# Optimization experiments

Measured on AMD Instinct MI355X. Metric: run time of the kernel, lower is better.

Reference implementation:

```python
import jax, jax.numpy as jnp
import numpy as np

N = 100000   # nodes
E = 1600000  # edges
R = 4        # relations (bond types)
D_IN = 38    # atom feature dim
H = 64       # hidden dim
G = 1000     # graphs in batch
O = 1        # output tasks


def layer_norm(h, g, b):
    mu = h.mean(-1, keepdims=True)
    var = ((h - mu) ** 2).mean(-1, keepdims=True)
    return (h - mu) / jnp.sqrt(var + 1e-5) * g + b


def rgcn_conv(x, src, dst, etype, W, root_w, bias):
    # PyG RGCNConv with aggr='mean': per-relation mean of neighbor features,
    # then per-relation linear transform (mean commutes with the linear map),
    # plus root transform and bias.
    msg = x[src]                                   # [E, F] gather (memory-bound)
    seg = dst * R + etype                          # fused (node, relation) segment id
    sums = jax.ops.segment_sum(msg, seg, num_segments=N * R)          # [N*R, F]
    cnt = jax.ops.segment_sum(jnp.ones((msg.shape[0],), x.dtype), seg,
                              num_segments=N * R)                     # [N*R]
    mean = sums / jnp.maximum(cnt, 1.0)[:, None]
    mean = mean.reshape(N, R, x.shape[-1])         # [N, R, F]
    return jnp.einsum('nri,rio->no', mean, W) + x @ root_w + bias


def setup_inputs() -> dict:
    key = jax.random.key(0)
    ks = jax.random.split(key, 32)
    s = lambda k, sh: (jax.random.normal(k, sh, jnp.float32) * 0.05)
    inp = {
        'x': jax.random.normal(ks[0], (N, D_IN), jnp.float32),
        'edge_index': jax.random.randint(ks[1], (2, E), 0, N),
        'edge_type': jax.random.randint(ks[2], (E,), 0, R),
        'batch': jnp.sort(jax.random.randint(ks[3], (N,), 0, G)),
        # layer 0 (D_IN -> H), with linear residual projection
        'W0': s(ks[4], (R, D_IN, H)), 'root0': s(ks[5], (D_IN, H)), 'b0': jnp.zeros((H,), jnp.float32),
        'ln0_g': jnp.ones((H,), jnp.float32), 'ln0_b': jnp.zeros((H,), jnp.float32),
        'res_w': s(ks[6], (D_IN, H)), 'res_b': jnp.zeros((H,), jnp.float32),
        # layer 1
        'W1': s(ks[7], (R, H, H)), 'root1': s(ks[8], (H, H)), 'b1': jnp.zeros((H,), jnp.float32),
        'ln1_g': jnp.ones((H,), jnp.float32), 'ln1_b': jnp.zeros((H,), jnp.float32),
        # layer 2
        'W2': s(ks[9], (R, H, H)), 'root2': s(ks[10], (H, H)), 'b2': jnp.zeros((H,), jnp.float32),
        'ln2_g': jnp.ones((H,), jnp.float32), 'ln2_b': jnp.zeros((H,), jnp.float32),
        # readout MLP
        'ro_w1': s(ks[11], (H, H)), 'ro_b1': jnp.zeros((H,), jnp.float32),
        'ro_w2': s(ks[12], (H, O)), 'ro_b2': jnp.zeros((O,), jnp.float32),
    }
    return inp


def reference(x, edge_index, edge_type, batch,
              W0, root0, b0, ln0_g, ln0_b, res_w, res_b,
              W1, root1, b1, ln1_g, ln1_b,
              W2, root2, b2, ln2_g, ln2_b,
              ro_w1, ro_b1, ro_w2, ro_b2):
    src, dst = edge_index[0], edge_index[1]
    # dropout is inference-mode (identity)
    h = jax.nn.relu(rgcn_conv(x, src, dst, edge_type, W0, root0, b0))
    x1 = layer_norm(h + x @ res_w + res_b, ln0_g, ln0_b)
    h = jax.nn.relu(rgcn_conv(x1, src, dst, edge_type, W1, root1, b1))
    x2 = layer_norm(h + x1, ln1_g, ln1_b)
    h = jax.nn.relu(rgcn_conv(x2, src, dst, edge_type, W2, root2, b2))
    x3 = layer_norm(h + x2, ln2_g, ln2_b)
    # global mean pool over graphs
    pooled = jax.ops.segment_sum(x3, batch, num_segments=G)
    cnt = jax.ops.segment_sum(jnp.ones((N,), x3.dtype), batch, num_segments=G)
    pooled = pooled / jnp.maximum(cnt, 1.0)[:, None]
    out = jax.nn.relu(pooled @ ro_w1 + ro_b1) @ ro_w2 + ro_b2  # [G, O]
    return out
```

## Files before the change

### kernel.cpp

```cpp
#include <hip/hip_runtime.h>
#include <math.h>

#define NNODES 100000
#define NEDGES 1600000
#define NREL   4
#define DIN    38
#define HID    64
#define NGRAPH 1000
#define NSEG   (NNODES * NREL)
#define NSCANB ((NSEG + 1023) / 1024)

__device__ __forceinline__ float wsum64(float v) {
    #pragma unroll
    for (int o = 32; o; o >>= 1) v += __shfl_xor(v, o);
    return v;
}

__device__ __forceinline__ void ln_group_reduce(float& s) {
    s += __shfl_xor(s, 1);
    s += __shfl_xor(s, 2);
    s += __shfl_xor(s, 4);
    s += __shfl_xor(s, 8);
}

__global__ __launch_bounds__(256) void count_kernel(
    const int* __restrict__ ei, const int* __restrict__ et,
    int* __restrict__ cnt) {
    int i = blockIdx.x * 256 + threadIdx.x;
    if (i < NEDGES) {
        int dst = ei[NEDGES + i];
        atomicAdd(&cnt[dst * NREL + et[i]], 1);
    }
}

__global__ __launch_bounds__(256) void scan1_kernel(
    const int* __restrict__ cnt, int* __restrict__ excl, int* __restrict__ bsum) {
    __shared__ int tmp[256];
    int tid = threadIdx.x;
    int base = blockIdx.x * 1024 + tid * 4;
    int v0 = 0, v1 = 0, v2 = 0, v3 = 0;
    if (base + 0 < NSEG) v0 = cnt[base + 0];
    if (base + 1 < NSEG) v1 = cnt[base + 1];
    if (base + 2 < NSEG) v2 = cnt[base + 2];
    if (base + 3 < NSEG) v3 = cnt[base + 3];
    int s = v0 + v1 + v2 + v3;
    tmp[tid] = s;
    __syncthreads();
    for (int off = 1; off < 256; off <<= 1) {
        int t = (tid >= off) ? tmp[tid - off] : 0;
        __syncthreads();
        tmp[tid] += t;
        __syncthreads();
    }
    if (tid == 255) bsum[blockIdx.x] = tmp[255];
    int run = tmp[tid] - s;
    if (base + 0 < NSEG) excl[base + 0] = run; run += v0;
    if (base + 1 < NSEG) excl[base + 1] = run; run += v1;
    if (base + 2 < NSEG) excl[base + 2] = run; run += v2;
    if (base + 3 < NSEG) excl[base + 3] = run;
}

__global__ __launch_bounds__(512) void scan2_kernel(int* __restrict__ bsum) {
    __shared__ int tmp[512];
    int tid = threadIdx.x;
    int v = (tid < NSCANB) ? bsum[tid] : 0;
    tmp[tid] = v;
    __syncthreads();
    for (int off = 1; off < 512; off <<= 1) {
        int t = (tid >= off) ? tmp[tid - off] : 0;
        __syncthreads();
        tmp[tid] += t;
        __syncthreads();
    }
    if (tid < NSCANB) bsum[tid] = tmp[tid] - v;
}

__global__ __launch_bounds__(256) void place_kernel(
    const int* __restrict__ ei, const int* __restrict__ et,
    const int* __restrict__ excl, const int* __restrict__ bsum,
    int* __restrict__ fill, int* __restrict__ esrc) {
    int e = blockIdx.x * 256 + threadIdx.x;
    if (e >= NEDGES) return;
    int r = et[e];
    int seg = ei[NEDGES + e] * NREL + r;
    int pos = excl[seg] + bsum[seg >> 10] + atomicAdd(&fill[seg], 1);
    esrc[pos] = ei[e] | (r << 20);
}

__global__ __launch_bounds__(256, 4) void gemm12_kernel(
    const float* __restrict__ x, const float* __restrict__ W,
    const float* __restrict__ root, float* __restrict__ y,
    float* __restrict__ yroot) {
    __shared__ float As[64][68];
    __shared__ float Ws[64][68];
    int tid = threadIdx.x;
    int nbase = blockIdx.x * 64;

    {
        int sk = tid & 63, sm0 = tid >> 6;
        #pragma unroll
        for (int mm = 0; mm < 16; ++mm) {
            int m = sm0 + mm * 4;
            int n = nbase + m; if (n > NNODES - 1) n = NNODES - 1;
            As[sk][m] = x[(size_t)n * 64 + sk];
        }
    }
    int r = tid >> 4, c = tid & 15;
    int scc = tid & 63, sk0 = tid >> 6;

    for (int nc = 0; nc < 5; ++nc) {
        __syncthreads();
        const float* src = (nc < 4) ? (W + nc * 4096) : root;
        #pragma unroll
        for (int kk = 0; kk < 16; ++kk) {
            int k = sk0 + kk * 4;
            Ws[k][scc] = src[k * 64 + scc];
        }
        __syncthreads();
        float acc[4][4] = {};
        #pragma unroll 4
        for (int k = 0; k < 64; ++k) {
            const float4 av = *(const float4*)&As[k][r * 4];
            const float4 wv = *(const float4*)&Ws[k][c * 4];
            const float a_[4] = {av.x, av.y, av.z, av.w};
            const float w_[4] = {wv.x, wv.y, wv.z, wv.w};
            #pragma unroll
            for (int i = 0; i < 4; ++i)
                #pragma unroll
                for (int j = 0; j < 4; ++j)
                    acc[i][j] += a_[i] * w_[j];
        }
        #pragma unroll
        for (int i = 0; i < 4; ++i) {
            int n = nbase + r * 4 + i;
            if (n < NNODES) {
                float4 o = make_float4(acc[i][0], acc[i][1], acc[i][2], acc[i][3]);
                if (nc < 4) *(float4*)&y[(size_t)n * 256 + nc * 64 + c * 4] = o;
                else        *(float4*)&yroot[(size_t)n * 64 + c * 4] = o;
            }
        }
    }
}

__global__ __launch_bounds__(256, 4) void gemm0_kernel(
    const float* __restrict__ x, const float* __restrict__ W0,
    const float* __restrict__ root0, const float* __restrict__ resw,
    float* __restrict__ y, float* __restrict__ yroot, float* __restrict__ xres) {
    __shared__ float As[38][68];
    __shared__ float Ws[38][68];
    int tid = threadIdx.x;
    int nbase = blockIdx.x * 64;

    for (int idx = tid; idx < 64 * 38; idx += 256) {
        int m = idx / 38, k = idx - m * 38;
        int n = nbase + m; if (n > NNODES - 1) n = NNODES - 1;
        As[k][m] = x[(size_t)n * DIN + k];
    }
    int r = tid >> 4, c = tid & 15;

    for (int nc = 0; nc < 6; ++nc) {
        __syncthreads();
        const float* src = (nc < 4) ? (W0 + nc * DIN * 64)
                                    : (nc == 4 ? root0 : resw);
        for (int idx = tid; idx < 38 * 64; idx += 256) {
            int k = idx >> 6, cc = idx & 63;
            Ws[k][cc] = src[idx];
        }
        __syncthreads();
        float acc[4][4] = {};
        #pragma unroll 2
        for (int k = 0; k < 38; ++k) {
            const float4 av = *(const float4*)&As[k][r * 4];
            const float4 wv = *(const float4*)&Ws[k][c * 4];
            const float a_[4] = {av.x, av.y, av.z, av.w};
            const float w_[4] = {wv.x, wv.y, wv.z, wv.w};
            #pragma unroll
            for (int i = 0; i < 4; ++i)
                #pragma unroll
                for (int j = 0; j < 4; ++j)
                    acc[i][j] += a_[i] * w_[j];
        }
        #pragma unroll
        for (int i = 0; i < 4; ++i) {
            int n = nbase + r * 4 + i;
            if (n < NNODES) {
                float4 o = make_float4(acc[i][0], acc[i][1], acc[i][2], acc[i][3]);
                if (nc < 4)      *(float4*)&y[(size_t)n * 256 + nc * 64 + c * 4] = o;
                else if (nc == 4) *(float4*)&yroot[(size_t)n * 64 + c * 4] = o;
                else             *(float4*)&xres[(size_t)n * 64 + c * 4] = o;
            }
        }
    }
}

template <bool L0>
__global__ __launch_bounds__(256, 8) void epi_kernel(
    const float* __restrict__ y, const float* __restrict__ yroot,
    const float* __restrict__ xprev,
    const int* __restrict__ esrc, const int* __restrict__ excl,
    const int* __restrict__ bsum, const int* __restrict__ cnt,
    const float* __restrict__ bias, const float* __restrict__ bias2,
    const float* __restrict__ lng, const float* __restrict__ lnb,
    float* __restrict__ dst) {
    int n = (blockIdx.x * 256 + threadIdx.x) >> 6;
    int lane = threadIdx.x & 63;
    if (n >= NNODES) return;
    int q = lane >> 4;
    int cl = lane & 15;

    int s4 = n * 4;
    int myc = 0, myb = 0;
    if (lane < 4) {
        myc = cnt[s4 + lane];
        myb = excl[s4 + lane] + bsum[(s4 + lane) >> 10];
    }
    float myi = 1.f / fmaxf((float)myc, 1.f);
    int c0 = __shfl(myc, 0), c1 = __shfl(myc, 1);
    int c2 = __shfl(myc, 2), c3 = __shfl(myc, 3);
    float i0 = __shfl(myi, 0), i1 = __shfl(myi, 1);
    float i2 = __shfl(myi, 2), i3 = __shfl(myi, 3);
    int beg = __shfl(myb, 0);
    int ctot = c0 + c1 + c2 + c3;

    float acc[4] = {0.f, 0.f, 0.f, 0.f};
    for (int base = 0; base < ctot; base += 64) {
        int rem = ctot - base; if (rem > 64) rem = 64;
        int raw = (lane < rem) ? esrc[beg + base + lane] : 0;
        int src = raw & 0xFFFFF;
        int rel = raw >> 20;
        int moff = src * 4 + rel;
        float ic = (rel & 2) ? ((rel & 1) ? i3 : i2)
                             : ((rel & 1) ? i1 : i0);
        if (lane >= rem) ic = 0.f;

        int it = (rem + 3) >> 2;
        int i = 0;
        for (; i + 4 <= it; i += 4) {
            int l0 = (i + 0) * 4 + q, l1 = (i + 1) * 4 + q;
            int l2 = (i + 2) * 4 + q, l3 = (i + 3) * 4 + q;
            int o0 = __shfl(moff, l0), o1 = __shfl(moff, l1);
            int o2 = __shfl(moff, l2), o3 = __shfl(moff, l3);
            float s0 = __shfl(ic, l0), s1 = __shfl(ic, l1);
            float s2 = __shfl(ic, l2), s3 = __shfl(ic, l3);
            const float4 v0 = *(const float4*)&y[(size_t)o0 * 64 + cl * 4];
            const float4 v1 = *(const float4*)&y[(size_t)o1 * 64 + cl * 4];
            const float4 v2 = *(const float4*)&y[(size_t)o2 * 64 + cl * 4];
            const float4 v3 = *(const float4*)&y[(size_t)o3 * 64 + cl * 4];
            acc[0] += v0.x * s0; acc[1] += v0.y * s0;
            acc[2] += v0.z * s0; acc[3] += v0.w * s0;
            acc[0] += v1.x * s1; acc[1] += v1.y * s1;
            acc[2] += v1.z * s1; acc[3] += v1.w * s1;
            acc[0] += v2.x * s2; acc[1] += v2.y * s2;
            acc[2] += v2.z * s2; acc[3] += v2.w * s2;
            acc[0] += v3.x * s3; acc[1] += v3.y * s3;
            acc[2] += v3.z * s3; acc[3] += v3.w * s3;
        }
        for (; i < it; ++i) {
            int l = i * 4 + q;
            int o = __shfl(moff, l);
            float sc = __shfl(ic, l);
            const float4 v = *(const float4*)&y[(size_t)o * 64 + cl * 4];
            acc[0] += v.x * sc; acc[1] += v.y * sc;
            acc[2] += v.z * sc; acc[3] += v.w * sc;
        }
    }
    #pragma unroll
    for (int j = 0; j < 4; ++j) {
        acc[j] += __shfl_xor(acc[j], 16);
        acc[j] += __shfl_xor(acc[j], 32);
    }

    const float4 yr = *(const float4*)&yroot[(size_t)n * 64 + cl * 4];
    const float4 bv = *(const float4*)&bias[cl * 4];
    const float4 rv = *(const float4*)&xprev[(size_t)n * 64 + cl * 4];
    const float y_[4] = {yr.x, yr.y, yr.z, yr.w};
    const float b_[4] = {bv.x, bv.y, bv.z, bv.w};
    const float r_[4] = {rv.x, rv.y, rv.z, rv.w};
    float u[4];
    float s = 0.f;
    #pragma unroll
    for (int j = 0; j < 4; ++j) {
        u[j] = fmaxf(acc[j] + y_[j] + b_[j], 0.f) + r_[j];
        s += u[j];
    }
    if (L0) {
        const float4 sv = *(const float4*)&bias2[cl * 4];
        const float s2_[4] = {sv.x, sv.y, sv.z, sv.w};
        #pragma unroll
        for (int j = 0; j < 4; ++j) { u[j] += s2_[j]; s += s2_[j]; }
    }
    ln_group_reduce(s);
    float mu = s * (1.f / 64.f);
    float qq = 0.f;
    #pragma unroll
    for (int j = 0; j < 4; ++j) { u[j] -= mu; qq += u[j] * u[j]; }
    ln_group_reduce(qq);
    float inv = 1.f / sqrtf(qq * (1.f / 64.f) + 1e-5f);
    const float4 gv = *(const float4*)&lng[cl * 4];
    const float4 ev = *(const float4*)&lnb[cl * 4];
    const float g_[4] = {gv.x, gv.y, gv.z, gv.w};
    const float e_[4] = {ev.x, ev.y, ev.z, ev.w};
    float oq = u[q] * inv * g_[q] + e_[q];
    dst[(size_t)n * 64 + cl * 4 + q] = oq;
}

__global__ __launch_bounds__(256) void readout_kernel(
    const float* __restrict__ xfin, const int* __restrict__ batch,
    const float* __restrict__ w1, const float* __restrict__ b1,
    const float* __restrict__ w2, const float* __restrict__ b2,
    float* __restrict__ out) {
    __shared__ float wl[64][64];
    int tid = threadIdx.x;
    for (int idx = tid; idx < 64 * 64; idx += 256) {
        wl[idx >> 6][idx & 63] = w1[idx];
    }
    __syncthreads();
    int wv = tid >> 6, lane = tid & 63;
    int g = blockIdx.x * 4 + wv;
    if (g >= NGRAPH) return;
    int lo = 0, hi = NNODES;
    while (lo < hi) { int mid = (lo + hi) >> 1; if (batch[mid] < g) lo = mid + 1; else hi = mid; }
    int lb = lo;
    hi = NNODES;
    while (lo < hi) { int mid = (lo + hi) >> 1; if (batch[mid] < g + 1) lo = mid + 1; else hi = mid; }
    int ub = lo;
    float s0 = 0.f, s1 = 0.f, s2 = 0.f, s3 = 0.f;
    int n2 = lb;
    for (; n2 + 4 <= ub; n2 += 4) {
        s0 += xfin[(size_t)(n2 + 0) * 64 + lane];
        s1 += xfin[(size_t)(n2 + 1) * 64 + lane];
        s2 += xfin[(size_t)(n2 + 2) * 64 + lane];
        s3 += xfin[(size_t)(n2 + 3) * 64 + lane];
    }
    for (; n2 < ub; ++n2) s0 += xfin[(size_t)n2 * 64 + lane];
    float p = (s0 + s1 + s2 + s3) / fmaxf((float)(ub - lb), 1.f);
    float acc = b1[lane];
    for (int f = 0; f < 64; ++f) {
        acc += __shfl(p, f) * wl[f][lane];
    }
    float t = fmaxf(acc, 0.f);
    float v = t * w2[lane];
    v = wsum64(v);
    if (lane == 0) out[g] = v + b2[0];
}

extern "C" void kernel_launch(void* const* d_in, const int* in_sizes, int n_in,
                              void* d_out, int out_size, void* d_ws, size_t ws_size,
                              hipStream_t stream) {
    const float* x     = (const float*)d_in[0];
    const int*   ei    = (const int*)d_in[1];
    const int*   et    = (const int*)d_in[2];
    const int*   batch = (const int*)d_in[3];
    const float* W0    = (const float*)d_in[4];
    const float* root0 = (const float*)d_in[5];
    const float* b0    = (const float*)d_in[6];
    const float* ln0g  = (const float*)d_in[7];
    const float* ln0b  = (const float*)d_in[8];
    const float* resw  = (const float*)d_in[9];
    const float* resb  = (const float*)d_in[10];
    const float* W1    = (const float*)d_in[11];
    const float* root1 = (const float*)d_in[12];
    const float* b1    = (const float*)d_in[13];
    const float* ln1g  = (const float*)d_in[14];
    const float* ln1b  = (const float*)d_in[15];
    const float* W2    = (const float*)d_in[16];
    const float* root2 = (const float*)d_in[17];
    const float* b2    = (const float*)d_in[18];
    const float* ln2g  = (const float*)d_in[19];
    const float* ln2b  = (const float*)d_in[20];
    const float* row1  = (const float*)d_in[21];
    const float* rob1  = (const float*)d_in[22];
    const float* row2  = (const float*)d_in[23];
    const float* rob2  = (const float*)d_in[24];
    float* out = (float*)d_out;

    char* ws = (char*)d_ws;
    size_t off = 0;
    int* cnt    = (int*)(ws + off); off += (size_t)NSEG * 4;
    int* fill   = (int*)(ws + off); off += (size_t)NSEG * 4;
    size_t zero_bytes = off;
    int* excl   = (int*)(ws + off); off += (size_t)NSEG * 4;
    int* bsum   = (int*)(ws + off); off += 4096;
    int* esrc   = (int*)(ws + off); off += (size_t)NEDGES * 4;
    float* y    = (float*)(ws + off); off += (size_t)NNODES * 256 * 4;
    float* yroot= (float*)(ws + off); off += (size_t)NNODES * 64 * 4;
    float* xA   = (float*)(ws + off); off += (size_t)NNODES * 64 * 4;
    float* xB   = (float*)(ws + off); off += (size_t)NNODES * 64 * 4;

    hipMemsetAsync(d_ws, 0, zero_bytes, stream);

    count_kernel<<<6250, 256, 0, stream>>>(ei, et, cnt);
    scan1_kernel<<<NSCANB, 256, 0, stream>>>(cnt, excl, bsum);
    scan2_kernel<<<1, 512, 0, stream>>>(bsum);
    place_kernel<<<6250, 256, 0, stream>>>(ei, et, excl, bsum, fill, esrc);

    const int GBLK = (NNODES + 63) / 64;
    const int EBLK = (NNODES + 3) / 4;

    gemm0_kernel<<<GBLK, 256, 0, stream>>>(x, W0, root0, resw, y, yroot, xA);
    epi_kernel<true><<<EBLK, 256, 0, stream>>>(
        y, yroot, xA, esrc, excl, bsum, cnt, b0, resb, ln0g, ln0b, xA);

    gemm12_kernel<<<GBLK, 256, 0, stream>>>(xA, W1, root1, y, yroot);
    epi_kernel<false><<<EBLK, 256, 0, stream>>>(
        y, yroot, xA, esrc, excl, bsum, cnt, b1, resb, ln1g, ln1b, xB);

    gemm12_kernel<<<GBLK, 256, 0, stream>>>(xB, W2, root2, y, yroot);
    epi_kernel<false><<<EBLK, 256, 0, stream>>>(
        y, yroot, xB, esrc, excl, bsum, cnt, b2, resb, ln2g, ln2b, xA);

    readout_kernel<<<250, 256, 0, stream>>>(
        xA, batch, row1, rob1, row2, rob2, out);
}
```

Measured before the change: 691.9 us.

## Store per-relation transformed features in bf16 and fuse edge counting with layer-0 GEMM

The per-relation transformed features y are now written as bf16 instead of fp32, halving the bytes gathered per edge in the memory-bound aggregation kernels. The edge-count pass is merged into the layer-0 GEMM launch as extra blocks, and it records each edge's atomic rank. The placement pass then reuses that rank instead of doing a second atomic on a fill array. This saves a launch and an atomic pass but adds a rank buffer and loses precision in the neighbour messages.

```diff
diff --git a/kernel.cpp b/kernel.cpp
--- a/kernel.cpp
+++ b/kernel.cpp
@@ -9,6 +9,7 @@
 #define NGRAPH 1000
 #define NSEG   (NNODES * NREL)
 #define NSCANB ((NSEG + 1023) / 1024)
+#define CBLK   6250
 
 __device__ __forceinline__ float wsum64(float v) {
     #pragma unroll
@@ -23,13 +24,81 @@
     s += __shfl_xor(s, 8);
 }
 
-__global__ __launch_bounds__(256) void count_kernel(
+__device__ __forceinline__ unsigned short f2bf(float f) {
+    unsigned u = __float_as_uint(f);
+    return (unsigned short)((u + 0x7FFFu + ((u >> 16) & 1u)) >> 16);
+}
+__device__ __forceinline__ float bf2f(unsigned short b) {
+    return __uint_as_float(((unsigned)b) << 16);
+}
+
+__global__ __launch_bounds__(256, 4) void fused0_kernel(
     const int* __restrict__ ei, const int* __restrict__ et,
-    int* __restrict__ cnt) {
-    int i = blockIdx.x * 256 + threadIdx.x;
-    if (i < NEDGES) {
-        int dst = ei[NEDGES + i];
-        atomicAdd(&cnt[dst * NREL + et[i]], 1);
+    int* __restrict__ cnt, int* __restrict__ rank,
+    const float* __restrict__ x, const float* __restrict__ W0,
+    const float* __restrict__ root0, const float* __restrict__ resw,
+    unsigned short* __restrict__ y, float* __restrict__ yroot,
+    float* __restrict__ xres) {
+    __shared__ float As[38][68];
+    __shared__ float Ws[38][68];
+
+    if (blockIdx.x < CBLK) {
+        int i = blockIdx.x * 256 + threadIdx.x;
+        if (i < NEDGES) {
+            int dst = ei[NEDGES + i];
+            rank[i] = atomicAdd(&cnt[dst * NREL + et[i]], 1);
+        }
+        return;
+    }
+
+    int tid = threadIdx.x;
+    int nbase = (blockIdx.x - CBLK) * 64;
+
+    for (int idx = tid; idx < 64 * 38; idx += 256) {
+        int m = idx / 38, k = idx - m * 38;
+        int n = nbase + m; if (n > NNODES - 1) n = NNODES - 1;
+        As[k][m] = x[(size_t)n * DIN + k];
+    }
+    int r = tid >> 4, c = tid & 15;
+
+    for (int nc = 0; nc < 6; ++nc) {
+        __syncthreads();
+        const float* src = (nc < 4) ? (W0 + nc * DIN * 64)
+                                    : (nc == 4 ? root0 : resw);
+        for (int idx = tid; idx < 38 * 64; idx += 256) {
+            int k = idx >> 6, cc = idx & 63;
+            Ws[k][cc] = src[idx];
+        }
+        __syncthreads();
+        float acc[4][4] = {};
+        #pragma unroll 2
+        for (int k = 0; k < 38; ++k) {
+            const float4 av = *(const float4*)&As[k][r * 4];
+            const float4 wv = *(const float4*)&Ws[k][c * 4];
+            const float a_[4] = {av.x, av.y, av.z, av.w};
+            const float w_[4] = {wv.x, wv.y, wv.z, wv.w};
+            #pragma unroll
+            for (int i = 0; i < 4; ++i)
+                #pragma unroll
+                for (int j = 0; j < 4; ++j)
+                    acc[i][j] += a_[i] * w_[j];
+        }
+        #pragma unroll
+        for (int i = 0; i < 4; ++i) {
+            int n = nbase + r * 4 + i;
+            if (n < NNODES) {
+                if (nc < 4) {
+                    ushort4 o;
+                    o.x = f2bf(acc[i][0]); o.y = f2bf(acc[i][1]);
+                    o.z = f2bf(acc[i][2]); o.w = f2bf(acc[i][3]);
+                    *(ushort4*)&y[(size_t)n * 256 + nc * 64 + c * 4] = o;
+                } else {
+                    float4 o = make_float4(acc[i][0], acc[i][1], acc[i][2], acc[i][3]);
+                    if (nc == 4) *(float4*)&yroot[(size_t)n * 64 + c * 4] = o;
+                    else         *(float4*)&xres[(size_t)n * 64 + c * 4] = o;
+                }
+            }
+        }
     }
 }
 
@@ -78,18 +147,18 @@
 __global__ __launch_bounds__(256) void place_kernel(
     const int* __restrict__ ei, const int* __restrict__ et,
     const int* __restrict__ excl, const int* __restrict__ bsum,
-    int* __restrict__ fill, int* __restrict__ esrc) {
+    const int* __restrict__ rank, int* __restrict__ esrc) {
     int e = blockIdx.x * 256 + threadIdx.x;
     if (e >= NEDGES) return;
     int r = et[e];
     int seg = ei[NEDGES + e] * NREL + r;
-    int pos = excl[seg] + bsum[seg >> 10] + atomicAdd(&fill[seg], 1);
+    int pos = excl[seg] + bsum[seg >> 10] + rank[e];
     esrc[pos] = ei[e] | (r << 20);
 }
 
 __global__ __launch_bounds__(256, 4) void gemm12_kernel(
     const float* __restrict__ x, const float* __restrict__ W,
-    const float* __restrict__ root, float* __restrict__ y,
+    const float* __restrict__ root, unsigned short* __restrict__ y,
     float* __restrict__ yroot) {
     __shared__ float As[64][68];
     __shared__ float Ws[64][68];
@@ -134,60 +203,15 @@
         for (int i = 0; i < 4; ++i) {
             int n = nbase + r * 4 + i;
             if (n < NNODES) {
-                float4 o = make_float4(acc[i][0], acc[i][1], acc[i][2], acc[i][3]);
-                if (nc < 4) *(float4*)&y[(size_t)n * 256 + nc * 64 + c * 4] = o;
-                else        *(float4*)&yroot[(size_t)n * 64 + c * 4] = o;
-            }
-        }
-    }
-}
-
-__global__ __launch_bounds__(256, 4) void gemm0_kernel(
-    const float* __restrict__ x, const float* __restrict__ W0,
-    const float* __restrict__ root0, const float* __restrict__ resw,
-    float* __restrict__ y, float* __restrict__ yroot, float* __restrict__ xres) {
-    __shared__ float As[38][68];
-    __shared__ float Ws[38][68];
-    int tid = threadIdx.x;
-    int nbase = blockIdx.x * 64;
-
-    for (int idx = tid; idx < 64 * 38; idx += 256) {
-        int m = idx / 38, k = idx - m * 38;
-        int n = nbase + m; if (n > NNODES - 1) n = NNODES - 1;
-        As[k][m] = x[(size_t)n * DIN + k];
-    }
-    int r = tid >> 4, c = tid & 15;
-
-    for (int nc = 0; nc < 6; ++nc) {
-        __syncthreads();
-        const float* src = (nc < 4) ? (W0 + nc * DIN * 64)
-                                    : (nc == 4 ? root0 : resw);
-        for (int idx = tid; idx < 38 * 64; idx += 256) {
-            int k = idx >> 6, cc = idx & 63;
-            Ws[k][cc] = src[idx];
-        }
-        __syncthreads();
-        float acc[4][4] = {};
-        #pragma unroll 2
-        for (int k = 0; k < 38; ++k) {
-            const float4 av = *(const float4*)&As[k][r * 4];
-            const float4 wv = *(const float4*)&Ws[k][c * 4];
-            const float a_[4] = {av.x, av.y, av.z, av.w};
-            const float w_[4] = {wv.x, wv.y, wv.z, wv.w};
-            #pragma unroll
-            for (int i = 0; i < 4; ++i)
-                #pragma unroll
-                for (int j = 0; j < 4; ++j)
-                    acc[i][j] += a_[i] * w_[j];
-        }
-        #pragma unroll
-        for (int i = 0; i < 4; ++i) {
-            int n = nbase + r * 4 + i;
-            if (n < NNODES) {
-                float4 o = make_float4(acc[i][0], acc[i][1], acc[i][2], acc[i][3]);
-                if (nc < 4)      *(float4*)&y[(size_t)n * 256 + nc * 64 + c * 4] = o;
-                else if (nc == 4) *(float4*)&yroot[(size_t)n * 64 + c * 4] = o;
-                else             *(float4*)&xres[(size_t)n * 64 + c * 4] = o;
+                if (nc < 4) {
+                    ushort4 o;
+                    o.x = f2bf(acc[i][0]); o.y = f2bf(acc[i][1]);
+                    o.z = f2bf(acc[i][2]); o.w = f2bf(acc[i][3]);
+                    *(ushort4*)&y[(size_t)n * 256 + nc * 64 + c * 4] = o;
+                } else {
+                    *(float4*)&yroot[(size_t)n * 64 + c * 4] =
+                        make_float4(acc[i][0], acc[i][1], acc[i][2], acc[i][3]);
+                }
             }
         }
     }
@@ -195,7 +219,7 @@
 
 template <bool L0>
 __global__ __launch_bounds__(256, 8) void epi_kernel(
-    const float* __restrict__ y, const float* __restrict__ yroot,
+    const unsigned short* __restrict__ y, const float* __restrict__ yroot,
     const float* __restrict__ xprev,
     const int* __restrict__ esrc, const int* __restrict__ excl,
     const int* __restrict__ bsum, const int* __restrict__ cnt,
@@ -242,26 +266,26 @@
             int o2 = __shfl(moff, l2), o3 = __shfl(moff, l3);
             float s0 = __shfl(ic, l0), s1 = __shfl(ic, l1);
             float s2 = __shfl(ic, l2), s3 = __shfl(ic, l3);
-            const float4 v0 = *(const float4*)&y[(size_t)o0 * 64 + cl * 4];
-            const float4 v1 = *(const float4*)&y[(size_t)o1 * 64 + cl * 4];
-            const float4 v2 = *(const float4*)&y[(size_t)o2 * 64 + cl * 4];
-            const float4 v3 = *(const float4*)&y[(size_t)o3 * 64 + cl * 4];
-            acc[0] += v0.x * s0; acc[1] += v0.y * s0;
-            acc[2] += v0.z * s0; acc[3] += v0.w * s0;
-            acc[0] += v1.x * s1; acc[1] += v1.y * s1;
-            acc[2] += v1.z * s1; acc[3] += v1.w * s1;
-            acc[0] += v2.x * s2; acc[1] += v2.y * s2;
-            acc[2] += v2.z * s2; acc[3] += v2.w * s2;
-            acc[0] += v3.x * s3; acc[1] += v3.y * s3;
-            acc[2] += v3.z * s3; acc[3] += v3.w * s3;
+            const ushort4 v0 = *(const ushort4*)&y[(size_t)o0 * 64 + cl * 4];
+            const ushort4 v1 = *(const ushort4*)&y[(size_t)o1 * 64 + cl * 4];
+            const ushort4 v2 = *(const ushort4*)&y[(size_t)o2 * 64 + cl * 4];
+            const ushort4 v3 = *(const ushort4*)&y[(size_t)o3 * 64 + cl * 4];
+            acc[0] += bf2f(v0.x) * s0; acc[1] += bf2f(v0.y) * s0;
+            acc[2] += bf2f(v0.z) * s0; acc[3] += bf2f(v0.w) * s0;
+            acc[0] += bf2f(v1.x) * s1; acc[1] += bf2f(v1.y) * s1;
+            acc[2] += bf2f(v1.z) * s1; acc[3] += bf2f(v1.w) * s1;
+            acc[0] += bf2f(v2.x) * s2; acc[1] += bf2f(v2.y) * s2;
+            acc[2] += bf2f(v2.z) * s2; acc[3] += bf2f(v2.w) * s2;
+            acc[0] += bf2f(v3.x) * s3; acc[1] += bf2f(v3.y) * s3;
+            acc[2] += bf2f(v3.z) * s3; acc[3] += bf2f(v3.w) * s3;
         }
         for (; i < it; ++i) {
             int l = i * 4 + q;
             int o = __shfl(moff, l);
             float sc = __shfl(ic, l);
-            const float4 v = *(const float4*)&y[(size_t)o * 64 + cl * 4];
-            acc[0] += v.x * sc; acc[1] += v.y * sc;
-            acc[2] += v.z * sc; acc[3] += v.w * sc;
+            const ushort4 v = *(const ushort4*)&y[(size_t)o * 64 + cl * 4];
+            acc[0] += bf2f(v.x) * sc; acc[1] += bf2f(v.y) * sc;
+            acc[2] += bf2f(v.z) * sc; acc[3] += bf2f(v.w) * sc;
         }
     }
     #pragma unroll
@@ -377,27 +401,29 @@
     char* ws = (char*)d_ws;
     size_t off = 0;
     int* cnt    = (int*)(ws + off); off += (size_t)NSEG * 4;
-    int* fill   = (int*)(ws + off); off += (size_t)NSEG * 4;
     size_t zero_bytes = off;
     int* excl   = (int*)(ws + off); off += (size_t)NSEG * 4;
     int* bsum   = (int*)(ws + off); off += 4096;
+    int* rank   = (int*)(ws + off); off += (size_t)NEDGES * 4;
     int* esrc   = (int*)(ws + off); off += (size_t)NEDGES * 4;
-    float* y    = (float*)(ws + off); off += (size_t)NNODES * 256 * 4;
+    unsigned short* y = (unsigned short*)(ws + off);
+    off += (size_t)NNODES * 256 * 2;
     float* yroot= (float*)(ws + off); off += (size_t)NNODES * 64 * 4;
     float* xA   = (float*)(ws + off); off += (size_t)NNODES * 64 * 4;
     float* xB   = (float*)(ws + off); off += (size_t)NNODES * 64 * 4;
 
     hipMemsetAsync(d_ws, 0, zero_bytes, stream);
 
-    count_kernel<<<6250, 256, 0, stream>>>(ei, et, cnt);
+    const int GBLK = (NNODES + 63) / 64;
+    const int EBLK = (NNODES + 3) / 4;
+
+    fused0_kernel<<<CBLK + GBLK, 256, 0, stream>>>(
+        ei, et, cnt, rank, x, W0, root0, resw, y, yroot, xA);
+
     scan1_kernel<<<NSCANB, 256, 0, stream>>>(cnt, excl, bsum);
     scan2_kernel<<<1, 512, 0, stream>>>(bsum);
-    place_kernel<<<6250, 256, 0, stream>>>(ei, et, excl, bsum, fill, esrc);
-
-    const int GBLK = (NNODES + 63) / 64;
-    const int EBLK = (NNODES + 3) / 4;
-
-    gemm0_kernel<<<GBLK, 256, 0, stream>>>(x, W0, root0, resw, y, yroot, xA);
+    place_kernel<<<6250, 256, 0, stream>>>(ei, et, excl, bsum, rank, esrc);
+
     epi_kernel<true><<<EBLK, 256, 0, stream>>>(
         y, yroot, xA, esrc, excl, bsum, cnt, b0, resb, ln0g, ln0b, xA);
 
```

After: 594.5 us. 14.1% less time.
